# Kernel tuning notes

Hardware: AMD Instinct MI355X
Metric: run time of the kernel (lower is better)

Reference implementation:

```python
import jax, jax.numpy as jnp
import numpy as np

BS, N, J, F = 8, 1024, 4, 32
N_CLASSES = 2


def setup_inputs() -> dict:
    key = jax.random.key(0)
    k1, k2, k3, k4 = jax.random.split(key, 4)
    WW = jax.random.normal(k1, (BS, N, N, J), dtype=jnp.float32)
    x = jax.random.normal(k2, (BS, N, F), dtype=jnp.float32)
    # nn.Linear(J*F, n_classes): weight (n_classes, J*F), bias (n_classes,)
    bound = 1.0 / np.sqrt(J * F)
    fc_w = jax.random.uniform(k3, (N_CLASSES, J * F), minval=-bound, maxval=bound, dtype=jnp.float32)
    fc_b = jax.random.uniform(k4, (N_CLASSES,), minval=-bound, maxval=bound, dtype=jnp.float32)
    return {"WW": WW, "x": x, "fc_w": fc_w, "fc_b": fc_b}


def reference(WW, x, fc_w, fc_b):
    bs, n, _, j = WW.shape
    f = x.shape[-1]
    # GMul: out[b,n,j*F+f] = sum_m W[b,n,m,j] * x[b,m,f]
    h = jnp.einsum('bnmj,bmf->bnjf', WW, x).reshape(bs, n, j * f)
    # Linear over last dim
    out = h @ fc_w.T + fc_b  # (bs, N, n_classes)
    return out
```

## Files before the change

### kernel.cpp

```cpp
#include <hip/hip_runtime.h>

#define BS 8
#define NN 1024
#define JJ 4
#define FF 32
#define NC 2

typedef float f4v __attribute__((ext_vector_type(4)));

__global__ void __launch_bounds__(256) compute_y_kernel(
    const float* __restrict__ x, const float* __restrict__ fc_w,
    float2* __restrict__ yA, float2* __restrict__ yB) {
    int idx = blockIdx.x * blockDim.x + threadIdx.x;
    if (idx >= BS * NN * JJ) return;
    int j  = idx & (JJ - 1);
    int bm = idx >> 2;
    const float* xr = x + (size_t)bm * FF;
    const float* w0 = fc_w + 0 * (JJ * FF) + j * FF;
    const float* w1 = fc_w + 1 * (JJ * FF) + j * FF;
    float a0 = 0.f, a1 = 0.f;
#pragma unroll
    for (int f = 0; f < FF; ++f) {
        float xv = xr[f];
        a0 += xv * w0[f];
        a1 += xv * w1[f];
    }
    float2 v = make_float2(a0, a1);
    if (j < 2) yA[bm * 2 + j]       = v;
    else       yB[bm * 2 + (j - 2)] = v;
}

__global__ void __launch_bounds__(256) reduce_out_kernel(
    const float* __restrict__ WW, const float4* __restrict__ yA,
    const float4* __restrict__ yB, const float* __restrict__ fc_b,
    float* __restrict__ out) {
    __shared__ float4 lyA[NN];
    __shared__ float4 lyB[NN];

    const int blk  = blockIdx.x;
    const int b    = blk >> 7;
    const int wave = threadIdx.x >> 6;
    const int lane = threadIdx.x & 63;

    for (int i = threadIdx.x; i < NN; i += 256) {
        lyA[i] = yA[(size_t)b * NN + i];
        lyB[i] = yB[(size_t)b * NN + i];
    }
    __syncthreads();

    const int row0 = blk * 8 + wave * 2;
    const f4v* W0 = reinterpret_cast<const f4v*>(WW) + (size_t)row0 * NN;
    const f4v* W1 = W0 + NN;

    float a00 = 0.f, a01 = 0.f, a10 = 0.f, a11 = 0.f;
#pragma unroll 4
    for (int m = lane; m < NN; m += 64) {
        f4v w0 = __builtin_nontemporal_load(W0 + m);
        f4v w1 = __builtin_nontemporal_load(W1 + m);
        float4 ya = lyA[m];
        float4 yb = lyB[m];
        a00 += w0.x * ya.x + w0.y * ya.z + w0.z * yb.x + w0.w * yb.z;
        a01 += w0.x * ya.y + w0.y * ya.w + w0.z * yb.y + w0.w * yb.w;
        a10 += w1.x * ya.x + w1.y * ya.z + w1.z * yb.x + w1.w * yb.z;
        a11 += w1.x * ya.y + w1.y * ya.w + w1.z * yb.y + w1.w * yb.w;
    }
#pragma unroll
    for (int off = 32; off > 0; off >>= 1) {
        a00 += __shfl_down(a00, off, 64);
        a01 += __shfl_down(a01, off, 64);
        a10 += __shfl_down(a10, off, 64);
        a11 += __shfl_down(a11, off, 64);
    }
    if (lane == 0) {
        float b0 = fc_b[0], b1 = fc_b[1];
        out[(size_t)row0 * NC + 0] = a00 + b0;
        out[(size_t)row0 * NC + 1] = a01 + b1;
        out[(size_t)(row0 + 1) * NC + 0] = a10 + b0;
        out[(size_t)(row0 + 1) * NC + 1] = a11 + b1;
    }
}

extern "C" void kernel_launch(void* const* d_in, const int* in_sizes, int n_in,
                              void* d_out, int out_size, void* d_ws, size_t ws_size,
                              hipStream_t stream) {
    const float* WW   = (const float*)d_in[0];
    const float* x    = (const float*)d_in[1];
    const float* fc_w = (const float*)d_in[2];
    const float* fc_b = (const float*)d_in[3];
    float* out = (float*)d_out;

    float* ws  = (float*)d_ws;
    float2* yA2 = (float2*)ws;
    float2* yB2 = (float2*)(ws + (size_t)BS * NN * 4);

    {
        int total = BS * NN * JJ;
        compute_y_kernel<<<(total + 255) / 256, 256, 0, stream>>>(x, fc_w, yA2, yB2);
    }
    {
        int blocks = (BS * NN) / 8;
        reduce_out_kernel<<<blocks, 256, 0, stream>>>(
            WW, (const float4*)yA2, (const float4*)yB2, fc_b, out);
    }
}
```

Before: 30.59 us.

## Fuse projection of x through fc_w into the WW reduction kernel

Removes the separate kernel that precomputed the x·fc_w projections into workspace. Each 1024-thread block now recomputes the projections for its whole batch into shared memory, then reduces 32 rows of WW against them. This saves a kernel launch and the workspace round trip, at the cost of redundant per-block recomputation, fewer and larger blocks, and a longer prologue before WW streaming begins. WW loads also switch from nontemporal to ordinary loads.

```diff
diff --git a/kernel.cpp b/kernel.cpp
--- a/kernel.cpp
+++ b/kernel.cpp
@@ -8,75 +8,75 @@
 
 typedef float f4v __attribute__((ext_vector_type(4)));
 
-__global__ void __launch_bounds__(256) compute_y_kernel(
-    const float* __restrict__ x, const float* __restrict__ fc_w,
-    float2* __restrict__ yA, float2* __restrict__ yB) {
-    int idx = blockIdx.x * blockDim.x + threadIdx.x;
-    if (idx >= BS * NN * JJ) return;
-    int j  = idx & (JJ - 1);
-    int bm = idx >> 2;
-    const float* xr = x + (size_t)bm * FF;
-    const float* w0 = fc_w + 0 * (JJ * FF) + j * FF;
-    const float* w1 = fc_w + 1 * (JJ * FF) + j * FF;
-    float a0 = 0.f, a1 = 0.f;
-#pragma unroll
-    for (int f = 0; f < FF; ++f) {
-        float xv = xr[f];
-        a0 += xv * w0[f];
-        a1 += xv * w1[f];
-    }
-    float2 v = make_float2(a0, a1);
-    if (j < 2) yA[bm * 2 + j]       = v;
-    else       yB[bm * 2 + (j - 2)] = v;
-}
-
-__global__ void __launch_bounds__(256) reduce_out_kernel(
-    const float* __restrict__ WW, const float4* __restrict__ yA,
-    const float4* __restrict__ yB, const float* __restrict__ fc_b,
+__global__ void __launch_bounds__(1024) fused_gmul_fc_kernel(
+    const float* __restrict__ WW, const float* __restrict__ x,
+    const float* __restrict__ fc_w, const float* __restrict__ fc_b,
     float* __restrict__ out) {
     __shared__ float4 lyA[NN];
     __shared__ float4 lyB[NN];
 
     const int blk  = blockIdx.x;
-    const int b    = blk >> 7;
-    const int wave = threadIdx.x >> 6;
-    const int lane = threadIdx.x & 63;
+    const int b    = blk >> 5;
+    const int tid  = threadIdx.x;
+    const int wave = tid >> 6;
+    const int lane = tid & 63;
 
-    for (int i = threadIdx.x; i < NN; i += 256) {
-        lyA[i] = yA[(size_t)b * NN + i];
-        lyB[i] = yB[(size_t)b * NN + i];
+    {
+        const float4* xr =
+            reinterpret_cast<const float4*>(x + ((size_t)b * NN + tid) * FF);
+        float xv[FF];
+#pragma unroll
+        for (int q = 0; q < FF / 4; ++q) {
+            float4 v = xr[q];
+            xv[q * 4 + 0] = v.x; xv[q * 4 + 1] = v.y;
+            xv[q * 4 + 2] = v.z; xv[q * 4 + 3] = v.w;
+        }
+        float a00 = 0.f, a01 = 0.f, a10 = 0.f, a11 = 0.f;
+        float a20 = 0.f, a21 = 0.f, a30 = 0.f, a31 = 0.f;
+        const float* w0 = fc_w;
+        const float* w1 = fc_w + JJ * FF;
+#pragma unroll
+        for (int f = 0; f < FF; ++f) {
+            float xf = xv[f];
+            a00 += xf * w0[0 * FF + f];  a01 += xf * w1[0 * FF + f];
+            a10 += xf * w0[1 * FF + f];  a11 += xf * w1[1 * FF + f];
+            a20 += xf * w0[2 * FF + f];  a21 += xf * w1[2 * FF + f];
+            a30 += xf * w0[3 * FF + f];  a31 += xf * w1[3 * FF + f];
+        }
+        lyA[tid] = make_float4(a00, a01, a10, a11);
+        lyB[tid] = make_float4(a20, a21, a30, a31);
     }
     __syncthreads();
 
-    const int row0 = blk * 8 + wave * 2;
+    const int row0 = blk * 32 + wave * 2;
     const f4v* W0 = reinterpret_cast<const f4v*>(WW) + (size_t)row0 * NN;
     const f4v* W1 = W0 + NN;
 
-    float a00 = 0.f, a01 = 0.f, a10 = 0.f, a11 = 0.f;
+    float s00 = 0.f, s01 = 0.f, s10 = 0.f, s11 = 0.f;
 #pragma unroll 4
     for (int m = lane; m < NN; m += 64) {
-        f4v w0 = __builtin_nontemporal_load(W0 + m);
-        f4v w1 = __builtin_nontemporal_load(W1 + m);
+        f4v w0 = W0[m];
+        f4v w1 = W1[m];
         float4 ya = lyA[m];
         float4 yb = lyB[m];
-        a00 += w0.x * ya.x + w0.y * ya.z + w0.z * yb.x + w0.w * yb.z;
-        a01 += w0.x * ya.y + w0.y * ya.w + w0.z * yb.y + w0.w * yb.w;
-        a10 += w1.x * ya.x + w1.y * ya.z + w1.z * yb.x + w1.w * yb.z;
-        a11 += w1.x * ya.y + w1.y * ya.w + w1.z * yb.y + w1.w * yb.w;
+        s00 += w0.x * ya.x + w0.y * ya.z + w0.z * yb.x + w0.w * yb.z;
+        s01 += w0.x * ya.y + w0.y * ya.w + w0.z * yb.y + w0.w * yb.w;
+        s10 += w1.x * ya.x + w1.y * ya.z + w1.z * yb.x + w1.w * yb.z;
+        s11 += w1.x * ya.y + w1.y * ya.w + w1.z * yb.y + w1.w * yb.w;
     }
 #pragma unroll
     for (int off = 32; off > 0; off >>= 1) {
-        a00 += __shfl_down(a00, off, 64);
-        a01 += __shfl_down(a01, off, 64);
-        a10 += __shfl_down(a10, off, 64);
-        a11 += __shfl_down(a11, off, 64);
+        s00 += __shfl_down(s00, off, 64);
+        s01 += __shfl_down(s01, off, 64);
+        s10 += __shfl_down(s10, off, 64);
+        s11 += __shfl_down(s11, off, 64);
     }
     if (lane == 0) {
         float b0 = fc_b[0], b1 = fc_b[1];
-        out[(size_t)row0 * NC + 0] = a00 + b0;
-        out[(size_t)row0 * NC + 1] = a01 + b1;
-        out[(size_t)(row0 + 1) * NC + 0] = a10 + b0;
-        out[(size_t)(row0 + 1) * NC + 1] = a11 + b1;
+        out[(size_t)row0 * NC + 0] = s00 + b0;
+        out[(size_t)row0 * NC + 1] = s01 + b1;
+        out[(size_t)(row0 + 1) * NC + 0] = s10 + b0;
+        out[(size_t)(row0 + 1) * NC + 1] = s11 + b1;
     }
 }
 
@@ -89,17 +89,6 @@
     const float* fc_b = (const float*)d_in[3];
     float* out = (float*)d_out;
 
-    float* ws  = (float*)d_ws;
-    float2* yA2 = (float2*)ws;
-    float2* yB2 = (float2*)(ws + (size_t)BS * NN * 4);
-
-    {
-        int total = BS * NN * JJ;
-        compute_y_kernel<<<(total + 255) / 256, 256, 0, stream>>>(x, fc_w, yA2, yB2);
-    }
-    {
-        int blocks = (BS * NN) / 8;
-        reduce_out_kernel<<<blocks, 256, 0, stream>>>(
-            WW, (const float4*)yA2, (const float4*)yB2, fc_b, out);
-    }
+    int blocks = (BS * NN) / 32;
+    fused_gmul_fc_kernel<<<blocks, 1024, 0, stream>>>(WW, x, fc_w, fc_b, out);
 }
```

Result: slower. 33.34 us (+9.0%).

## Stream each block's rows as one contiguous chunk with block-wide partial reduction

Applied to the files above, without the earlier changes.

The reduction kernel now has all 256 threads read one contiguous 8-row span of WW in order, one float4 per thread per step, instead of each wave reading two rows. Per-row sums are reduced inside each wave, staged in shared memory and combined across the four waves. Loads switch from nontemporal to regular, and launch bounds request 4 blocks per CU. This is meant to give fully coalesced, sequential streaming of the large WW tensor, at the cost of extra shuffle reductions and a second barrier.

```diff
diff --git a/kernel.cpp b/kernel.cpp
--- a/kernel.cpp
+++ b/kernel.cpp
@@ -5,6 +5,9 @@
 #define JJ 4
 #define FF 32
 #define NC 2
+
+#define ROWS 8
+#define THREADS 256
 
 typedef float f4v __attribute__((ext_vector_type(4)));
 
@@ -30,53 +33,56 @@
     else       yB[bm * 2 + (j - 2)] = v;
 }
 
-__global__ void __launch_bounds__(256) reduce_out_kernel(
+__global__ void __launch_bounds__(THREADS, 4) reduce_seq_kernel(
     const float* __restrict__ WW, const float4* __restrict__ yA,
     const float4* __restrict__ yB, const float* __restrict__ fc_b,
     float* __restrict__ out) {
     __shared__ float4 lyA[NN];
     __shared__ float4 lyB[NN];
+    __shared__ float2 part[ROWS][4];
 
-    const int blk  = blockIdx.x;
-    const int b    = blk >> 7;
-    const int wave = threadIdx.x >> 6;
-    const int lane = threadIdx.x & 63;
+    const int tid  = threadIdx.x;
+    const int wave = tid >> 6;
+    const int lane = tid & 63;
+    const int rowbase = blockIdx.x * ROWS;
+    const int b       = rowbase >> 10;
 
-    for (int i = threadIdx.x; i < NN; i += 256) {
+    for (int i = tid; i < NN; i += THREADS) {
         lyA[i] = yA[(size_t)b * NN + i];
         lyB[i] = yB[(size_t)b * NN + i];
     }
     __syncthreads();
 
-    const int row0 = blk * 8 + wave * 2;
-    const f4v* W0 = reinterpret_cast<const f4v*>(WW) + (size_t)row0 * NN;
-    const f4v* W1 = W0 + NN;
+    const f4v* Wp = reinterpret_cast<const f4v*>(WW) + (size_t)rowbase * NN;
 
-    float a00 = 0.f, a01 = 0.f, a10 = 0.f, a11 = 0.f;
-#pragma unroll 4
-    for (int m = lane; m < NN; m += 64) {
-        f4v w0 = __builtin_nontemporal_load(W0 + m);
-        f4v w1 = __builtin_nontemporal_load(W1 + m);
+    float s0 = 0.f, s1 = 0.f;
+#pragma unroll
+    for (int k = 0; k < 4 * ROWS; ++k) {
+        const int m = ((k & 3) << 8) + tid;
+        f4v w = Wp[(size_t)k * THREADS + tid];
         float4 ya = lyA[m];
         float4 yb = lyB[m];
-        a00 += w0.x * ya.x + w0.y * ya.z + w0.z * yb.x + w0.w * yb.z;
-        a01 += w0.x * ya.y + w0.y * ya.w + w0.z * yb.y + w0.w * yb.w;
-        a10 += w1.x * ya.x + w1.y * ya.z + w1.z * yb.x + w1.w * yb.z;
-        a11 += w1.x * ya.y + w1.y * ya.w + w1.z * yb.y + w1.w * yb.w;
+        s0 += w.x * ya.x + w.y * ya.z + w.z * yb.x + w.w * yb.z;
+        s1 += w.x * ya.y + w.y * ya.w + w.z * yb.y + w.w * yb.w;
+        if ((k & 3) == 3) {
+#pragma unroll
+            for (int off = 32; off > 0; off >>= 1) {
+                s0 += __shfl_down(s0, off, 64);
+                s1 += __shfl_down(s1, off, 64);
+            }
+            if (lane == 0) part[k >> 2][wave] = make_float2(s0, s1);
+            s0 = 0.f; s1 = 0.f;
+        }
     }
-#pragma unroll
-    for (int off = 32; off > 0; off >>= 1) {
-        a00 += __shfl_down(a00, off, 64);
-        a01 += __shfl_down(a01, off, 64);
-        a10 += __shfl_down(a10, off, 64);
-        a11 += __shfl_down(a11, off, 64);
-    }
-    if (lane == 0) {
-        float b0 = fc_b[0], b1 = fc_b[1];
-        out[(size_t)row0 * NC + 0] = a00 + b0;
-        out[(size_t)row0 * NC + 1] = a01 + b1;
-        out[(size_t)(row0 + 1) * NC + 0] = a10 + b0;
-        out[(size_t)(row0 + 1) * NC + 1] = a11 + b1;
+    __syncthreads();
+
+    if (tid < ROWS) {
+        float2 p0 = part[tid][0], p1 = part[tid][1];
+        float2 p2 = part[tid][2], p3 = part[tid][3];
+        float2 r;
+        r.x = p0.x + p1.x + p2.x + p3.x + fc_b[0];
+        r.y = p0.y + p1.y + p2.y + p3.y + fc_b[1];
+        reinterpret_cast<float2*>(out)[rowbase + tid] = r;
     }
 }
 
@@ -89,7 +95,7 @@
     const float* fc_b = (const float*)d_in[3];
     float* out = (float*)d_out;
 
-    float* ws  = (float*)d_ws;
+    float* ws   = (float*)d_ws;
     float2* yA2 = (float2*)ws;
     float2* yB2 = (float2*)(ws + (size_t)BS * NN * 4);
 
@@ -98,8 +104,8 @@
         compute_y_kernel<<<(total + 255) / 256, 256, 0, stream>>>(x, fc_w, yA2, yB2);
     }
     {
-        int blocks = (BS * NN) / 8;
-        reduce_out_kernel<<<blocks, 256, 0, stream>>>(
+        int blocks = (BS * NN) / ROWS;
+        reduce_seq_kernel<<<blocks, THREADS, 0, stream>>>(
             WW, (const float4*)yA2, (const float4*)yB2, fc_b, out);
     }
 }
```

Result: slower. 31.46 us (+2.9%).
